# Optimization experiments

Measured on AMD Instinct MI355X. Metric: run time of the kernel, lower is better.

The kernel has to match this reference:

```python
import jax, jax.numpy as jnp
import numpy as np

B, T, C = 4, 2048, 1024
H = 16
D = C // H  # 64


def setup_inputs() -> dict:
    key = jax.random.key(0)
    ks = jax.random.split(key, 5)
    scale = 0.02
    x = jax.random.normal(ks[0], (B, T, C), dtype=jnp.float32)
    # Linear weights stored in [in, out] layout (equivalent to torch W.T)
    W_qkv = jax.random.normal(ks[1], (C, 3 * C), dtype=jnp.float32) * scale
    b_qkv = jax.random.normal(ks[2], (3 * C,), dtype=jnp.float32) * scale
    W_out = jax.random.normal(ks[3], (C, C), dtype=jnp.float32) * scale
    b_out = jax.random.normal(ks[4], (C,), dtype=jnp.float32) * scale
    return {"x": x, "W_qkv": W_qkv, "b_qkv": b_qkv, "W_out": W_out, "b_out": b_out}


def reference(x, W_qkv, b_qkv, W_out, b_out):
    Bx, Tx, Cx = x.shape
    qkv = x @ W_qkv + b_qkv                      # [B,T,3C]
    qkv = qkv.reshape(Bx, Tx, 3, H, D)
    q = jnp.transpose(qkv[:, :, 0], (0, 2, 1, 3))  # [B,H,T,D]
    k = jnp.transpose(qkv[:, :, 1], (0, 2, 1, 3))
    v = jnp.transpose(qkv[:, :, 2], (0, 2, 1, 3))
    scores = jnp.einsum('bhqd,bhkd->bhqk', q, k) / jnp.sqrt(jnp.float32(D))
    causal = jnp.tril(jnp.ones((Tx, Tx), dtype=bool))  # keep lower triangle
    scores = jnp.where(causal, scores, jnp.float32(-jnp.inf))
    w = jax.nn.softmax(scores, axis=-1)           # dropout p=0.0 (eval)
    out = jnp.einsum('bhqk,bhkd->bhqd', w, v)     # [B,H,T,D]
    out = jnp.transpose(out, (0, 2, 1, 3)).reshape(Bx, Tx, Cx)
    return out @ W_out + b_out
```

## Files before the change

### kernel.cpp

```cpp
#include <hip/hip_runtime.h>

typedef _Float16 f16;
typedef _Float16 f16x4 __attribute__((ext_vector_type(4)));
typedef _Float16 f16x8 __attribute__((ext_vector_type(8)));
typedef float    f32x4 __attribute__((ext_vector_type(4)));

#define B_ 4
#define T_ 2048
#define C_ 1024
#define H_ 16
#define D_ 64

__device__ __forceinline__ void gload_lds16(const f16* g, f16* l) {
  __builtin_amdgcn_global_load_lds(
      (const __attribute__((address_space(1))) unsigned int*)g,
      (__attribute__((address_space(3))) unsigned int*)l, 16, 0, 0);
}

__global__ void cvt_kernel(const float* __restrict__ in, f16* __restrict__ out, int n4) {
  int i = blockIdx.x * blockDim.x + threadIdx.x;
  int stride = gridDim.x * blockDim.x;
  for (; i < n4; i += stride) {
    float4 v = ((const float4*)in)[i];
    f16x4 h = { (f16)v.x, (f16)v.y, (f16)v.z, (f16)v.w };
    ((f16x4*)out)[i] = h;
  }
}

__global__ void transpose_cvt_kernel(const float* __restrict__ W, f16* __restrict__ Wt,
                                     int K, int N) {
  __shared__ f16 tile[32][33];
  int bx = blockIdx.x, by = blockIdx.y;
  int tx = threadIdx.x & 31, ty = threadIdx.x >> 5;
  #pragma unroll
  for (int i = ty; i < 32; i += 8)
    tile[i][tx] = (f16)W[(size_t)(by * 32 + i) * N + bx * 32 + tx];
  __syncthreads();
  #pragma unroll
  for (int i = ty; i < 32; i += 8)
    Wt[(size_t)(bx * 32 + i) * K + by * 32 + tx] = tile[tx][i];
}

template <int EPI>
__global__ __launch_bounds__(256, 2)
void gemm_kernel(const f16* __restrict__ A, const f16* __restrict__ Bt,
                 const float* __restrict__ bias, float* __restrict__ outF,
                 f16* __restrict__ q, f16* __restrict__ kk, f16* __restrict__ vt,
                 int M, int N, int K) {
  __shared__ __align__(16) f16 As[2][128 * 32];
  __shared__ __align__(16) f16 Bs[2][128 * 32];
  const int nbn = N >> 7;
  const int bid = blockIdx.x;
  const int bm = bid / nbn, bn = bid % nbn;
  const int m0 = bm << 7, n0 = bn << 7;
  const int tid = threadIdx.x;
  const int lane = tid & 63, wid = tid >> 6;
  const int wr = wid >> 1, wc = wid & 1;

  f32x4 acc[4][4] = {};

  const int srow = lane >> 2;
  const int scol = (lane & 3) << 3;
  const f16* Abase = A + (size_t)(m0 + srow) * K + scol;
  const f16* Bbase = Bt + (size_t)(n0 + srow) * K + scol;

  auto stage = [&](int buf, int kt) {
    const int c0 = wid * 2;
    #pragma unroll
    for (int c = c0; c < c0 + 2; ++c) {
      gload_lds16(Abase + (size_t)c * 16 * K + kt * 32, &As[buf][c * 512]);
      gload_lds16(Bbase + (size_t)c * 16 * K + kt * 32, &Bs[buf][c * 512]);
    }
  };

  const int ko = (lane >> 4) << 3;
  const int rr = lane & 15;

  auto compute = [&](int buf) {
    f16x8 af[4], bf[4];
    #pragma unroll
    for (int t = 0; t < 4; ++t) {
      af[t] = *(const f16x8*)&As[buf][(wr * 64 + t * 16 + rr) * 32 + ko];
      bf[t] = *(const f16x8*)&Bs[buf][(wc * 64 + t * 16 + rr) * 32 + ko];
    }
    #pragma unroll
    for (int i = 0; i < 4; ++i)
      #pragma unroll
      for (int j = 0; j < 4; ++j)
        acc[i][j] = __builtin_amdgcn_mfma_f32_16x16x32_f16(af[i], bf[j], acc[i][j], 0, 0, 0);
  };

  const int nk = K >> 5;
  int cur = 0;
  stage(0, 0);
  __syncthreads();
  for (int kt = 0; kt < nk; ++kt) {
    if (kt + 1 < nk) stage(cur ^ 1, kt + 1);
    compute(cur);
    __syncthreads();
    cur ^= 1;
  }

  const int col = lane & 15;
  const int row4 = (lane >> 4) << 2;
  #pragma unroll
  for (int i = 0; i < 4; ++i) {
    #pragma unroll
    for (int j = 0; j < 4; ++j) {
      const int n = n0 + wc * 64 + j * 16 + col;
      const float bn_ = bias[n];
      #pragma unroll
      for (int r = 0; r < 4; ++r) {
        const int m = m0 + wr * 64 + i * 16 + row4 + r;
        const float v = acc[i][j][r] + bn_;
        if (EPI == 1) {
          outF[(size_t)m * N + n] = v;
        } else {
          const int which = n >> 10;
          const int cc = n & 1023;
          const int h = cc >> 6, d = cc & 63;
          const int b = m >> 11, t = m & 2047;
          const size_t bh = (size_t)b * 16 + h;
          const f16 hv = (f16)v;
          if (which == 0)      q [(bh * T_ + t) * D_ + d] = hv;
          else if (which == 1) kk[(bh * T_ + t) * D_ + d] = hv;
          else                 vt[(bh * D_ + d) * T_ + t] = hv;
        }
      }
    }
  }
}

__global__ __launch_bounds__(512, 2)
void attn_kernel(const f16* __restrict__ Q, const f16* __restrict__ Kg,
                 const f16* __restrict__ Vt, f16* __restrict__ Aout) {
  __shared__ __align__(16) f16 Ks[2][64 * 64];
  __shared__ __align__(16) f16 Vs[2][64 * 64];
  __shared__ __align__(16) f16 Pt[8][16][72];

  const int bid = blockIdx.x;
  const int wgid = (bid & 7) * 128 + (bid >> 3);
  const int bh = wgid >> 4;
  const int ti = 15 - (wgid & 15);
  const int lane = threadIdx.x & 63, w = threadIdx.x >> 6;
  const int col = lane & 15;
  const int g = lane >> 4;
  const int ko = g << 3;

  const f16* Qp = Q + (size_t)bh * T_ * D_;
  const f16* Kp = Kg + (size_t)bh * T_ * D_;
  const f16* Vp = Vt + (size_t)bh * D_ * T_;

  const int srow8 = lane >> 3;
  const int scb = ((lane & 7) << 4) ^ (srow8 << 4);
  const int krow_s = (w << 3) + srow8;

  auto stage = [&](int buf, int kb) {
    gload_lds16(Kp + (size_t)(kb + krow_s) * D_ + (scb >> 1), &Ks[buf][w * 512]);
    gload_lds16(Vp + (size_t)krow_s * T_ + kb + (scb >> 1), &Vs[buf][w * 512]);
  };
  auto ldsK = [&](int buf, int krow, int d0) -> f16x8 {
    const int off = krow * 128 + ((d0 << 1) ^ ((krow & 7) << 4));
    return *(const f16x8*)((const char*)&Ks[buf][0] + off);
  };
  auto ldsV = [&](int buf, int drow, int k0) -> f16x8 {
    const int off = drow * 128 + ((k0 << 1) ^ ((drow & 7) << 4));
    return *(const f16x8*)((const char*)&Vs[buf][0] + off);
  };

  const int q0 = ti << 7;
  const int qrow0 = q0 + (w << 4);
  const int nkt = (ti << 1) + 2;
  const int qg = qrow0 + col;

  f16x8 qf[2];
  #pragma unroll
  for (int s = 0; s < 2; ++s) {
    f16x8 t = *(const f16x8*)&Qp[(size_t)qg * D_ + s * 32 + ko];
    #pragma unroll
    for (int e = 0; e < 8; ++e) t[e] = t[e] * (f16)0.125f;
    qf[s] = t;
  }

  f32x4 o[4] = {};
  float m = -1e30f, l = 0.f;

  stage(0, 0);
  __syncthreads();
  int cur = 0;
  for (int kt = 0; kt < nkt; ++kt) {
    const int kb = kt << 6;
    if (kt + 1 < nkt) stage(cur ^ 1, (kt + 1) << 6);

    if (kb <= qrow0 + 15) {
      f32x4 sc[4] = {};
      #pragma unroll
      for (int s = 0; s < 2; ++s)
        #pragma unroll
        for (int mt = 0; mt < 4; ++mt) {
          f16x8 kf = ldsK(cur, mt * 16 + col, s * 32 + ko);
          sc[mt] = __builtin_amdgcn_mfma_f32_16x16x32_f16(kf, qf[s], sc[mt], 0, 0, 0);
        }

      const bool needMask = (kb + 63 > qrow0);
      if (needMask) {
        #pragma unroll
        for (int mt = 0; mt < 4; ++mt)
          #pragma unroll
          for (int r = 0; r < 4; ++r)
            if (kb + mt * 16 + (g << 2) + r > qg) sc[mt][r] = -1e30f;
      }

      float mx = fmaxf(fmaxf(fmaxf(sc[0][0], sc[0][1]), fmaxf(sc[0][2], sc[0][3])),
                       fmaxf(fmaxf(sc[1][0], sc[1][1]), fmaxf(sc[1][2], sc[1][3])));
      mx = fmaxf(mx, fmaxf(fmaxf(fmaxf(sc[2][0], sc[2][1]), fmaxf(sc[2][2], sc[2][3])),
                           fmaxf(fmaxf(sc[3][0], sc[3][1]), fmaxf(sc[3][2], sc[3][3]))));
      mx = fmaxf(mx, __shfl_xor(mx, 16, 64));
      mx = fmaxf(mx, __shfl_xor(mx, 32, 64));

      if (!__all(mx - m <= 8.f)) {
        const float mnew = fmaxf(m, mx);
        const float alpha = __expf(m - mnew);
        m = mnew;
        l *= alpha;
        #pragma unroll
        for (int mt = 0; mt < 4; ++mt)
          #pragma unroll
          for (int r = 0; r < 4; ++r) o[mt][r] *= alpha;
      }

      float rs = 0.f;
      #pragma unroll
      for (int mt = 0; mt < 4; ++mt) {
        f16x4 ph;
        #pragma unroll
        for (int r = 0; r < 4; ++r) {
          const float p = __expf(sc[mt][r] - m);
          rs += p;
          ph[r] = (f16)p;
        }
        *(f16x4*)&Pt[w][col][mt * 16 + (g << 2)] = ph;
      }
      rs += __shfl_xor(rs, 16, 64);
      rs += __shfl_xor(rs, 32, 64);
      l += rs;

      #pragma unroll
      for (int s = 0; s < 2; ++s) {
        f16x8 pb = *(const f16x8*)&Pt[w][col][s * 32 + ko];
        #pragma unroll
        for (int mt = 0; mt < 4; ++mt) {
          f16x8 vf = ldsV(cur, mt * 16 + col, s * 32 + ko);
          o[mt] = __builtin_amdgcn_mfma_f32_16x16x32_f16(vf, pb, o[mt], 0, 0, 0);
        }
      }
    }

    __syncthreads();
    cur ^= 1;
  }

  const int b = bh >> 4, h = bh & 15;
  const float inv = 1.0f / l;
  const size_t rowoff = ((size_t)b * T_ + qg) * C_ + (size_t)h * D_;
  #pragma unroll
  for (int mt = 0; mt < 4; ++mt) {
    f16x4 ov;
    #pragma unroll
    for (int r = 0; r < 4; ++r) ov[r] = (f16)(o[mt][r] * inv);
    *(f16x4*)&Aout[rowoff + mt * 16 + (g << 2)] = ov;
  }
}

extern "C" void kernel_launch(void* const* d_in, const int* in_sizes, int n_in,
                              void* d_out, int out_size, void* d_ws, size_t ws_size,
                              hipStream_t stream) {
  const float* x    = (const float*)d_in[0];
  const float* Wqkv = (const float*)d_in[1];
  const float* bqkv = (const float*)d_in[2];
  const float* Wout = (const float*)d_in[3];
  const float* bout = (const float*)d_in[4];
  float* out = (float*)d_out;

  char* ws = (char*)d_ws;
  f16* xb     = (f16*)ws;
  f16* Wqkv_t = (f16*)(ws + (16u << 20));
  f16* Wout_t = (f16*)(ws + (22u << 20));
  f16* Qb     = (f16*)(ws + (24u << 20));
  f16* Kb     = (f16*)(ws + (40u << 20));
  f16* Vtb    = (f16*)(ws + (56u << 20));

  cvt_kernel<<<2048, 256, 0, stream>>>(x, xb, (B_ * T_ * C_) / 4);
  dim3 g1(3072 / 32, 1024 / 32);
  transpose_cvt_kernel<<<g1, 256, 0, stream>>>(Wqkv, Wqkv_t, 1024, 3072);
  dim3 g2(1024 / 32, 1024 / 32);
  transpose_cvt_kernel<<<g2, 256, 0, stream>>>(Wout, Wout_t, 1024, 1024);

  gemm_kernel<0><<<64 * 24, 256, 0, stream>>>(xb, Wqkv_t, bqkv, nullptr,
                                              Qb, Kb, Vtb, 8192, 3072, 1024);
  attn_kernel<<<1024, 512, 0, stream>>>(Qb, Kb, Vtb, xb );
  gemm_kernel<1><<<64 * 8, 256, 0, stream>>>(xb, Wout_t, bout, out,
                                             nullptr, nullptr, nullptr, 8192, 1024, 1024);
}
```

Baseline: 227.2 us.

## Triple-buffer GEMM LDS pipeline with XOR swizzle and raised MFMA priority

Moves the projection GEMM from double to triple buffering of the A/B LDS tiles, keeping two global-to-LDS loads in flight, with explicit vmcnt waits and raw barriers replacing __syncthreads. It adds an XOR swizzle on the 16-byte chunk index within each 64-byte row to reduce LDS bank conflicts on the fragment reads, and raises wave priority around the MFMA block. Launch bounds go from 2 to 3 blocks per CU. The intent is to hide global load latency and LDS conflicts; in exchange LDS use per block rises and register pressure may tighten under the higher occupancy target.

```diff
diff --git a/kernel.cpp b/kernel.cpp
--- a/kernel.cpp
+++ b/kernel.cpp
@@ -42,13 +42,13 @@
 }
 
 template <int EPI>
-__global__ __launch_bounds__(256, 2)
+__global__ __launch_bounds__(256, 3)
 void gemm_kernel(const f16* __restrict__ A, const f16* __restrict__ Bt,
                  const float* __restrict__ bias, float* __restrict__ outF,
                  f16* __restrict__ q, f16* __restrict__ kk, f16* __restrict__ vt,
                  int M, int N, int K) {
-  __shared__ __align__(16) f16 As[2][128 * 32];
-  __shared__ __align__(16) f16 Bs[2][128 * 32];
+  __shared__ __align__(16) f16 As[3][128 * 32];
+  __shared__ __align__(16) f16 Bs[3][128 * 32];
   const int nbn = N >> 7;
   const int bid = blockIdx.x;
   const int bm = bid / nbn, bn = bid % nbn;
@@ -60,7 +60,7 @@
   f32x4 acc[4][4] = {};
 
   const int srow = lane >> 2;
-  const int scol = (lane & 3) << 3;
+  const int scol = (((lane & 3) ^ ((lane >> 2) & 3)) << 3);
   const f16* Abase = A + (size_t)(m0 + srow) * K + scol;
   const f16* Bbase = Bt + (size_t)(n0 + srow) * K + scol;
 
@@ -73,32 +73,43 @@
     }
   };
 
-  const int ko = (lane >> 4) << 3;
+  const int g = lane >> 4;
   const int rr = lane & 15;
+  const int swz = (g ^ (rr & 3)) << 4;
 
   auto compute = [&](int buf) {
     f16x8 af[4], bf[4];
     #pragma unroll
     for (int t = 0; t < 4; ++t) {
-      af[t] = *(const f16x8*)&As[buf][(wr * 64 + t * 16 + rr) * 32 + ko];
-      bf[t] = *(const f16x8*)&Bs[buf][(wc * 64 + t * 16 + rr) * 32 + ko];
-    }
+      af[t] = *(const f16x8*)((const char*)&As[buf][0] + (wr * 64 + t * 16 + rr) * 64 + swz);
+      bf[t] = *(const f16x8*)((const char*)&Bs[buf][0] + (wc * 64 + t * 16 + rr) * 64 + swz);
+    }
+    __builtin_amdgcn_s_setprio(1);
     #pragma unroll
     for (int i = 0; i < 4; ++i)
       #pragma unroll
       for (int j = 0; j < 4; ++j)
         acc[i][j] = __builtin_amdgcn_mfma_f32_16x16x32_f16(af[i], bf[j], acc[i][j], 0, 0, 0);
+    __builtin_amdgcn_s_setprio(0);
   };
 
   const int nk = K >> 5;
-  int cur = 0;
+  int bcur = 0, bnext = 1, bnn = 2;
   stage(0, 0);
-  __syncthreads();
-  for (int kt = 0; kt < nk; ++kt) {
-    if (kt + 1 < nk) stage(cur ^ 1, kt + 1);
-    compute(cur);
-    __syncthreads();
-    cur ^= 1;
+  stage(1, 1);
+  asm volatile("s_waitcnt vmcnt(4)" ::: "memory");
+  __builtin_amdgcn_s_barrier();
+  __builtin_amdgcn_sched_barrier(0);
+  for (int t = 0; t < nk; ++t) {
+    if (t + 2 < nk) stage(bnn, t + 2);
+    compute(bcur);
+    if (t + 1 < nk) {
+      if (t + 2 < nk) asm volatile("s_waitcnt vmcnt(4)" ::: "memory");
+      else            asm volatile("s_waitcnt vmcnt(0)" ::: "memory");
+      __builtin_amdgcn_s_barrier();
+      __builtin_amdgcn_sched_barrier(0);
+    }
+    const int tmp = bcur; bcur = bnext; bnext = bnn; bnn = tmp;
   }
 
   const int col = lane & 15;
```

Measured after the change: 227.7 us. Within noise of the previous version (+0.2%).
